# Kernel tuning notes

Hardware: AMD Instinct MI355X
Metric: run time of the kernel (lower is better)

Reference implementation:

```python
import jax, jax.numpy as jnp
import numpy as np

H = 32  # LSTM hidden size (hardcoded in module)
N = 2 * H  # attention feature dim = 64


def setup_inputs() -> dict:
    key = jax.random.key(0)
    ks = jax.random.split(key, 16)
    B, T = 4096, 512
    inp = {
        "y_t_1_embed": jax.random.normal(ks[0], (B, 1), jnp.float32),
        "h0": jax.random.normal(ks[1], (1, B, H), jnp.float32),
        "c0": jax.random.normal(ks[2], (1, B, H), jnp.float32),
        "encoder_outputs": jax.random.normal(ks[3], (B, T, N), jnp.float32),
        "encoder_feature": jax.random.normal(ks[4], (B * T, N), jnp.float32),
        # LSTM params (PyTorch layout: gates ordered i, f, g, o)
        "W_ih": jax.random.normal(ks[5], (4 * H, 1), jnp.float32) * 0.1,
        "W_hh": jax.random.normal(ks[6], (4 * H, H), jnp.float32) * 0.1,
        "b_ih": jax.random.normal(ks[7], (4 * H,), jnp.float32) * 0.1,
        "b_hh": jax.random.normal(ks[8], (4 * H,), jnp.float32) * 0.1,
        # attention params
        "W_proj": jax.random.normal(ks[9], (N, N), jnp.float32) * 0.1,
        "b_proj": jax.random.normal(ks[10], (N,), jnp.float32) * 0.1,
        "v_w": jax.random.normal(ks[11], (N,), jnp.float32) * 0.1,
        # output MLP params
        "W1": jax.random.normal(ks[12], (N, 2 * N), jnp.float32) * 0.1,
        "b1": jax.random.normal(ks[13], (N,), jnp.float32) * 0.1,
        "W2": jax.random.normal(ks[14], (1, N), jnp.float32) * 0.1,
        "b2": jax.random.normal(ks[15], (1,), jnp.float32) * 0.1,
    }
    return inp


def _decoder_fwd(y, h0, c0, enc_out, enc_feat,
                 W_ih, W_hh, b_ih, b_hh, W_proj, b_proj, v_w, W1, b1, W2, b2):
    B, T, n = enc_out.shape
    h, c = h0[0], c0[0]  # [B, H]
    # single LSTM step (seq_len == 1)
    gates = y @ W_ih.T + h @ W_hh.T + (b_ih + b_hh)  # [B, 4H]
    i, f, g, o = jnp.split(gates, 4, axis=-1)
    c_new = jax.nn.sigmoid(f) * c + jax.nn.sigmoid(i) * jnp.tanh(g)
    h_new = jax.nn.sigmoid(o) * jnp.tanh(c_new)
    s_t_hat = jnp.concatenate([h_new, c_new], axis=1)  # [B, 2H]
    # additive (Bahdanau) attention
    dec_fea = s_t_hat @ W_proj.T + b_proj  # [B, N]
    e = jnp.tanh(enc_feat.reshape(B, T, n) + dec_fea[:, None, :])  # [B, T, N]
    scores = jnp.einsum("btn,n->bt", e, v_w)
    attn = jax.nn.softmax(scores, axis=-1)  # [B, T]
    c_t = jnp.einsum("bt,btn->bn", attn, enc_out)  # [B, N]
    # output MLP
    out_in = jnp.concatenate([s_t_hat, c_t], axis=1)  # [B, 2N]
    output = (out_in @ W1.T + b1) @ W2.T + b2  # [B, 1]
    return output, h_new[None], c_new[None]


def reference(y_t_1_embed, h0, c0, encoder_outputs, encoder_feature,
              W_ih, W_hh, b_ih, b_hh, W_proj, b_proj, v_w, W1, b1, W2, b2):
    return _decoder_fwd(y_t_1_embed, h0, c0, encoder_outputs, encoder_feature,
                        W_ih, W_hh, b_ih, b_hh, W_proj, b_proj, v_w, W1, b1, W2, b2)
```

## Files before the change

### kernel.cpp

```cpp
#include <hip/hip_runtime.h>

#define HH 32
#define NN 64
#define TMAX 512

#define BAR() do { asm volatile("s_waitcnt lgkmcnt(0)" ::: "memory"); \
                   __builtin_amdgcn_s_barrier(); } while (0)

__device__ __forceinline__ float ftanh(float x) {
    float a = __builtin_amdgcn_exp2f(x * 2.885390082f);
    float r = __builtin_amdgcn_rcpf(a + 1.0f);
    return __builtin_fmaf(-2.0f, r, 1.0f);
}
__device__ __forceinline__ float fsigmoid(float x) {
    float a = __builtin_amdgcn_exp2f(x * -1.442695041f);
    return __builtin_amdgcn_rcpf(1.0f + a);
}
__device__ __forceinline__ float fexp(float x) {
    return __builtin_amdgcn_exp2f(x * 1.442695041f);
}
__device__ __forceinline__ float rowsum16(float x) {
    int t;
    t = __builtin_amdgcn_update_dpp(0, __float_as_int(x), 0x128, 0xF, 0xF, true); x += __int_as_float(t);
    t = __builtin_amdgcn_update_dpp(0, __float_as_int(x), 0x124, 0xF, 0xF, true); x += __int_as_float(t);
    t = __builtin_amdgcn_update_dpp(0, __float_as_int(x), 0x122, 0xF, 0xF, true); x += __int_as_float(t);
    t = __builtin_amdgcn_update_dpp(0, __float_as_int(x), 0x121, 0xF, 0xF, true); x += __int_as_float(t);
    return x;
}

__global__ __launch_bounds__(256) void decoder_fused(
    const float* __restrict__ y, const float* __restrict__ h0, const float* __restrict__ c0,
    const float* __restrict__ enc_out, const float* __restrict__ enc_feat,
    const float* __restrict__ W_ih, const float* __restrict__ W_hh,
    const float* __restrict__ b_ih, const float* __restrict__ b_hh,
    const float* __restrict__ W_proj, const float* __restrict__ b_proj,
    const float* __restrict__ v_w,
    const float* __restrict__ W1, const float* __restrict__ b1,
    const float* __restrict__ W2, const float* __restrict__ b2,
    float* __restrict__ out, int B, int T)
{
    const int b   = blockIdx.x;
    const int tid = threadIdx.x;
    const int tg  = tid >> 4;
    const int nc  = tid & 15;
    const int n0  = nc * 4;

    __shared__ float s_h[HH];
    __shared__ float s_cstate[HH];
    __shared__ float s_gates[4 * HH];
    __shared__ float s_outin[2 * NN];
    __shared__ float s_decfea[NN];
    __shared__ float s_vw[NN];
    __shared__ float s_e[TMAX];
    __shared__ float s_ct[16 * NN];
    __shared__ float s_l[16];

    const float4* ef = (const float4*)(enc_feat + (size_t)b * T * NN);
    const float4* eo = (const float4*)(enc_out  + (size_t)b * T * NN);

    float4 fb0 = ef[(  0 + tg) * 16 + nc];
    float4 fb1 = ef[( 16 + tg) * 16 + nc];
    float4 fb2 = ef[( 32 + tg) * 16 + nc];
    float4 fb3 = ef[( 48 + tg) * 16 + nc];
    float4 ob0 = eo[(  0 + tg) * 16 + nc];
    float4 ob1 = eo[( 16 + tg) * 16 + nc];
    float4 ob2 = eo[( 32 + tg) * 16 + nc];
    float4 ob3 = eo[( 48 + tg) * 16 + nc];

    if (tid < HH) {
        s_h[tid]      = h0[(size_t)b * HH + tid];
        s_cstate[tid] = c0[(size_t)b * HH + tid];
    }
    if (tid >= 64 && tid < 128) s_vw[tid - 64] = v_w[tid - 64];
    BAR();

    if (tid < 4 * HH) {
        float acc = y[b] * W_ih[tid] + b_ih[tid] + b_hh[tid];
        const float* wr = W_hh + tid * HH;
        #pragma unroll
        for (int k = 0; k < HH; ++k) acc += wr[k] * s_h[k];
        s_gates[tid] = acc;
    }
    BAR();

    if (tid < HH) {
        float ig = fsigmoid(s_gates[tid]);
        float fg = fsigmoid(s_gates[HH + tid]);
        float gg = ftanh(s_gates[2 * HH + tid]);
        float og = fsigmoid(s_gates[3 * HH + tid]);
        float cn = fg * s_cstate[tid] + ig * gg;
        float hn = og * ftanh(cn);
        s_outin[tid]      = hn;
        s_outin[HH + tid] = cn;
        out[(size_t)B + (size_t)b * HH + tid]                  = hn;
        out[(size_t)B + (size_t)B * HH + (size_t)b * HH + tid] = cn;
    }
    BAR();

    if (tid < NN) {
        float acc = b_proj[tid];
        const float* wr = W_proj + tid * NN;
        #pragma unroll
        for (int k = 0; k < NN; ++k) acc += wr[k] * s_outin[k];
        s_decfea[tid] = acc;
    }
    BAR();

    const float vw0 = s_vw[n0], vw1 = s_vw[n0 + 1], vw2 = s_vw[n0 + 2], vw3 = s_vw[n0 + 3];
    const float df0 = s_decfea[n0], df1 = s_decfea[n0 + 1], df2 = s_decfea[n0 + 2], df3 = s_decfea[n0 + 3];

    #define PROCB(U, T_) do { \
        float p = vw0 * ftanh((U).x + df0) + vw1 * ftanh((U).y + df1) \
                + vw2 * ftanh((U).z + df2) + vw3 * ftanh((U).w + df3); \
        p = rowsum16(p); \
        float e = fexp(p); \
        lsum += e; \
        if (nc == 0) s_e[T_] = e; \
    } while (0)

    const int CMAX = T >> 6;
    float lsum = 0.0f;
    #pragma unroll 1
    for (int c = 0; c < CMAX - 1; ++c) {
        const int t0 = c * 64;
        { float4 u = fb0; fb0 = ef[(t0 +  64 + tg) * 16 + nc]; PROCB(u, t0 +      tg); }
        { float4 u = fb1; fb1 = ef[(t0 +  80 + tg) * 16 + nc]; PROCB(u, t0 + 16 + tg); }
        { float4 u = fb2; fb2 = ef[(t0 +  96 + tg) * 16 + nc]; PROCB(u, t0 + 32 + tg); }
        { float4 u = fb3; fb3 = ef[(t0 + 112 + tg) * 16 + nc]; PROCB(u, t0 + 48 + tg); }
    }
    {
        const int t0 = (CMAX - 1) * 64;
        PROCB(fb0, t0 +      tg);
        PROCB(fb1, t0 + 16 + tg);
        PROCB(fb2, t0 + 32 + tg);
        PROCB(fb3, t0 + 48 + tg);
    }
    if (nc == 0) s_l[tg] = lsum;

    #define PROCC(V, T_) do { \
        float e = s_e[T_]; \
        ax += e * (V).x; ay += e * (V).y; az += e * (V).z; aw += e * (V).w; \
    } while (0)

    float ax = 0.f, ay = 0.f, az = 0.f, aw = 0.f;
    #pragma unroll 1
    for (int c = 0; c < CMAX - 1; ++c) {
        const int t0 = c * 64;
        { float4 v = ob0; ob0 = eo[(t0 +  64 + tg) * 16 + nc]; PROCC(v, t0 +      tg); }
        { float4 v = ob1; ob1 = eo[(t0 +  80 + tg) * 16 + nc]; PROCC(v, t0 + 16 + tg); }
        { float4 v = ob2; ob2 = eo[(t0 +  96 + tg) * 16 + nc]; PROCC(v, t0 + 32 + tg); }
        { float4 v = ob3; ob3 = eo[(t0 + 112 + tg) * 16 + nc]; PROCC(v, t0 + 48 + tg); }
    }
    {
        const int t0 = (CMAX - 1) * 64;
        PROCC(ob0, t0 +      tg);
        PROCC(ob1, t0 + 16 + tg);
        PROCC(ob2, t0 + 32 + tg);
        PROCC(ob3, t0 + 48 + tg);
    }
    s_ct[tg * NN + n0]     = ax;
    s_ct[tg * NN + n0 + 1] = ay;
    s_ct[tg * NN + n0 + 2] = az;
    s_ct[tg * NN + n0 + 3] = aw;
    BAR();

    if (tid < NN) {
        float num = 0.0f, L = 0.0f;
        #pragma unroll
        for (int g = 0; g < 16; ++g) { num += s_ct[g * NN + tid]; L += s_l[g]; }
        s_outin[NN + tid] = num / L;
    }
    BAR();

    float v2 = 0.0f;
    if (tid < NN) {
        float acc = b1[tid];
        const float* wr = W1 + tid * 2 * NN;
        #pragma unroll
        for (int k = 0; k < 2 * NN; ++k) acc += wr[k] * s_outin[k];
        v2 = acc * W2[tid];
    }
    if (tid < 64) {
        #pragma unroll
        for (int mask = 32; mask >= 1; mask >>= 1) v2 += __shfl_xor(v2, mask);
        if (tid == 0) out[b] = v2 + b2[0];
    }
}

extern "C" void kernel_launch(void* const* d_in, const int* in_sizes, int n_in,
                              void* d_out, int out_size, void* d_ws, size_t ws_size,
                              hipStream_t stream) {
    const float* y        = (const float*)d_in[0];
    const float* h0       = (const float*)d_in[1];
    const float* c0       = (const float*)d_in[2];
    const float* enc_out  = (const float*)d_in[3];
    const float* enc_feat = (const float*)d_in[4];
    const float* W_ih     = (const float*)d_in[5];
    const float* W_hh     = (const float*)d_in[6];
    const float* b_ih     = (const float*)d_in[7];
    const float* b_hh     = (const float*)d_in[8];
    const float* W_proj   = (const float*)d_in[9];
    const float* b_proj   = (const float*)d_in[10];
    const float* v_w      = (const float*)d_in[11];
    const float* W1       = (const float*)d_in[12];
    const float* b1       = (const float*)d_in[13];
    const float* W2       = (const float*)d_in[14];
    const float* b2       = (const float*)d_in[15];
    float* out = (float*)d_out;

    const int B = in_sizes[0];
    const int T = in_sizes[3] / (B * NN);

    decoder_fused<<<B, 256, 0, stream>>>(
        y, h0, c0, enc_out, enc_feat, W_ih, W_hh, b_ih, b_hh,
        W_proj, b_proj, v_w, W1, b1, W2, b2, out, B, T);
}
```

Before: 192.2 us.

## Fuse score and context passes into a single streaming loop

Merges the two sequential passes, one computing attention weights and one accumulating the weighted encoder outputs, into a single loop. Each row's exp weight is applied immediately to the matching enc_out row, which removes the shared s_e buffer and its stores and loads. Both input streams are now prefetched together, so more loads are in flight per iteration, at the cost of more live registers. The kernel is bound by streaming two 512 MB inputs, so the change mainly affects how well their memory traffic overlaps.

```diff
diff --git a/kernel.cpp b/kernel.cpp
--- a/kernel.cpp
+++ b/kernel.cpp
@@ -2,7 +2,6 @@
 
 #define HH 32
 #define NN 64
-#define TMAX 512
 
 #define BAR() do { asm volatile("s_waitcnt lgkmcnt(0)" ::: "memory"); \
                    __builtin_amdgcn_s_barrier(); } while (0)
@@ -51,7 +50,6 @@
     __shared__ float s_outin[2 * NN];
     __shared__ float s_decfea[NN];
     __shared__ float s_vw[NN];
-    __shared__ float s_e[TMAX];
     __shared__ float s_ct[16 * NN];
     __shared__ float s_l[16];
 
@@ -59,12 +57,12 @@
     const float4* eo = (const float4*)(enc_out  + (size_t)b * T * NN);
 
     float4 fb0 = ef[(  0 + tg) * 16 + nc];
+    float4 ob0 = eo[(  0 + tg) * 16 + nc];
     float4 fb1 = ef[( 16 + tg) * 16 + nc];
+    float4 ob1 = eo[( 16 + tg) * 16 + nc];
     float4 fb2 = ef[( 32 + tg) * 16 + nc];
+    float4 ob2 = eo[( 32 + tg) * 16 + nc];
     float4 fb3 = ef[( 48 + tg) * 16 + nc];
-    float4 ob0 = eo[(  0 + tg) * 16 + nc];
-    float4 ob1 = eo[( 16 + tg) * 16 + nc];
-    float4 ob2 = eo[( 32 + tg) * 16 + nc];
     float4 ob3 = eo[( 48 + tg) * 16 + nc];
 
     if (tid < HH) {
@@ -109,59 +107,44 @@
     const float vw0 = s_vw[n0], vw1 = s_vw[n0 + 1], vw2 = s_vw[n0 + 2], vw3 = s_vw[n0 + 3];
     const float df0 = s_decfea[n0], df1 = s_decfea[n0 + 1], df2 = s_decfea[n0 + 2], df3 = s_decfea[n0 + 3];
 
-    #define PROCB(U, T_) do { \
+    float ax = 0.f, ay = 0.f, az = 0.f, aw = 0.f, lsum = 0.f;
+
+    #define PROC(U, V) do { \
         float p = vw0 * ftanh((U).x + df0) + vw1 * ftanh((U).y + df1) \
                 + vw2 * ftanh((U).z + df2) + vw3 * ftanh((U).w + df3); \
         p = rowsum16(p); \
         float e = fexp(p); \
         lsum += e; \
-        if (nc == 0) s_e[T_] = e; \
+        ax += e * (V).x; ay += e * (V).y; az += e * (V).z; aw += e * (V).w; \
     } while (0)
 
     const int CMAX = T >> 6;
-    float lsum = 0.0f;
     #pragma unroll 1
     for (int c = 0; c < CMAX - 1; ++c) {
         const int t0 = c * 64;
-        { float4 u = fb0; fb0 = ef[(t0 +  64 + tg) * 16 + nc]; PROCB(u, t0 +      tg); }
-        { float4 u = fb1; fb1 = ef[(t0 +  80 + tg) * 16 + nc]; PROCB(u, t0 + 16 + tg); }
-        { float4 u = fb2; fb2 = ef[(t0 +  96 + tg) * 16 + nc]; PROCB(u, t0 + 32 + tg); }
-        { float4 u = fb3; fb3 = ef[(t0 + 112 + tg) * 16 + nc]; PROCB(u, t0 + 48 + tg); }
-    }
-    {
-        const int t0 = (CMAX - 1) * 64;
-        PROCB(fb0, t0 +      tg);
-        PROCB(fb1, t0 + 16 + tg);
-        PROCB(fb2, t0 + 32 + tg);
-        PROCB(fb3, t0 + 48 + tg);
-    }
-    if (nc == 0) s_l[tg] = lsum;
-
-    #define PROCC(V, T_) do { \
-        float e = s_e[T_]; \
-        ax += e * (V).x; ay += e * (V).y; az += e * (V).z; aw += e * (V).w; \
-    } while (0)
-
-    float ax = 0.f, ay = 0.f, az = 0.f, aw = 0.f;
-    #pragma unroll 1
-    for (int c = 0; c < CMAX - 1; ++c) {
-        const int t0 = c * 64;
-        { float4 v = ob0; ob0 = eo[(t0 +  64 + tg) * 16 + nc]; PROCC(v, t0 +      tg); }
-        { float4 v = ob1; ob1 = eo[(t0 +  80 + tg) * 16 + nc]; PROCC(v, t0 + 16 + tg); }
-        { float4 v = ob2; ob2 = eo[(t0 +  96 + tg) * 16 + nc]; PROCC(v, t0 + 32 + tg); }
-        { float4 v = ob3; ob3 = eo[(t0 + 112 + tg) * 16 + nc]; PROCC(v, t0 + 48 + tg); }
-    }
-    {
-        const int t0 = (CMAX - 1) * 64;
-        PROCC(ob0, t0 +      tg);
-        PROCC(ob1, t0 + 16 + tg);
-        PROCC(ob2, t0 + 32 + tg);
-        PROCC(ob3, t0 + 48 + tg);
-    }
+        { float4 u = fb0, v = ob0;
+          fb0 = ef[(t0 +  64 + tg) * 16 + nc]; ob0 = eo[(t0 +  64 + tg) * 16 + nc];
+          PROC(u, v); }
+        { float4 u = fb1, v = ob1;
+          fb1 = ef[(t0 +  80 + tg) * 16 + nc]; ob1 = eo[(t0 +  80 + tg) * 16 + nc];
+          PROC(u, v); }
+        { float4 u = fb2, v = ob2;
+          fb2 = ef[(t0 +  96 + tg) * 16 + nc]; ob2 = eo[(t0 +  96 + tg) * 16 + nc];
+          PROC(u, v); }
+        { float4 u = fb3, v = ob3;
+          fb3 = ef[(t0 + 112 + tg) * 16 + nc]; ob3 = eo[(t0 + 112 + tg) * 16 + nc];
+          PROC(u, v); }
+    }
+    PROC(fb0, ob0);
+    PROC(fb1, ob1);
+    PROC(fb2, ob2);
+    PROC(fb3, ob3);
+
     s_ct[tg * NN + n0]     = ax;
     s_ct[tg * NN + n0 + 1] = ay;
     s_ct[tg * NN + n0 + 2] = az;
     s_ct[tg * NN + n0 + 3] = aw;
+    if (nc == 0) s_l[tg] = lsum;
     BAR();
 
     if (tid < NN) {
```

Measured after the change: 194.3 us. About the same (+1.1%).
